# Performance work log

Measured on AMD Instinct MI355X. Metric: run time of the kernel, lower is better.

## Reference

```python
import jax, jax.numpy as jnp
import numpy as np
from jax import lax

EPS = 1e-7  # keras.backend.epsilon()
DT = 0.05

def _k(a):
    # (3,3) -> HWIO (3,3,1,1) fp32 kernel constant
    return jnp.asarray(np.asarray(a, dtype=np.float32).reshape(3, 3, 1, 1))

KXP = _k([[0,0,0],[0,-1,1],[0,0,0]])
KXN = _k([[0,0,0],[-1,1,0],[0,0,0]])
KYP = _k([[0,1,0],[0,-1,0],[0,0,0]])
KYN = _k([[0,0,0],[0,1,0],[0,-1,0]])
KXC = _k([[0,0,0],[-1,0,1],[0,0,0]])
KYC = _k([[0,1,0],[0,0,0],[0,-1,0]])
KLX = _k([[1,0,-1],[2,0,-2],[1,0,-1]])
KLY = _k([[1,2,1],[0,0,0],[-1,-2,-1]])

def conv(x, k):
    # TF K.conv2d 'same' == XLA cross-correlation, NHWC/HWIO
    return lax.conv_general_dilated(x, k, (1, 1), 'SAME',
                                    dimension_numbers=('NHWC', 'HWIO', 'NHWC'))

def setup_inputs() -> dict:
    key = jax.random.key(0)
    k1, k2 = jax.random.split(key)
    B, H, W = 32, 512, 512
    u = jax.random.normal(k1, (B, H, W, 1), dtype=jnp.float32)
    img = jax.random.uniform(k2, (B, H, W, 1), dtype=jnp.float32)
    alpha = jnp.ones((1, 1, 1, 1), jnp.float32)
    beta = jnp.ones((1, 1, 1, 1), jnp.float32)
    gamma = jnp.ones((1, 1, 1, 1), jnp.float32)
    return {"u": u, "img": img, "alpha": alpha, "beta": beta, "gamma": gamma}

def reference(u, img, alpha, beta, gamma):
    # --- edge stopping function g(img) (precomputed in build() in original) ---
    ex = conv(img, KLX)
    ey = conv(img, KLY)
    edges = jnp.square(jnp.square(ex) + jnp.square(ey))
    edges = edges / jnp.max(edges)
    edges = 1.0 / (edges + 1.0)
    gex = conv(edges, KXC)
    gey = conv(edges, KYC)
    # --- upwind transport term ---
    xp = conv(u, KXP); xn = conv(u, KXN)
    yp = conv(u, KYP); yn = conv(u, KYN)
    fxp = jax.nn.relu(gex); fxn = -jax.nn.relu(-gex)
    fyp = jax.nn.relu(gey); fyn = -jax.nn.relu(-gey)
    transport = 20.0 * ((fxp * xp + fxn * xn) + (fyp * yp + fyn * yn))
    # --- curvature (divergence of normalized gradient) ---
    gux = conv(u, KXC)
    guy = conv(u, KYC)
    normu = jnp.sqrt(jnp.square(gux) + jnp.square(guy) + EPS)
    kappa = conv(gux / (normu + EPS), KXC) + conv(guy / (normu + EPS), KYC)
    curvature = edges * kappa * normu
    balloon = edges * normu
    return u + DT * (curvature * alpha + transport * beta + balloon * gamma)
```

## Files before the change

### kernel.cpp

```cpp
#include <hip/hip_runtime.h>

#define HH 512
#define WW 512
#define NB 32
#define EPSF 1e-7f
#define DTF 0.05f
#define RS1 4
#define RSF 8
#define PANW 256

__device__ __forceinline__ float bperm(int addr, float v) {
    return __int_as_float(__builtin_amdgcn_ds_bpermute(addr, __float_as_int(v)));
}

struct R10 { float v[10]; };

__device__ __forceinline__ void load_row10(const float* __restrict__ base, int row,
                                           int lane, int bpu, int bpd,
                                           bool lo, bool hi, R10& r) {
    if ((unsigned)row < (unsigned)HH) {
        const float4* p = (const float4*)(base + row * WW + 8 * lane);
        float4 a = p[0], b = p[1];
        r.v[1] = a.x; r.v[2] = a.y; r.v[3] = a.z; r.v[4] = a.w;
        r.v[5] = b.x; r.v[6] = b.y; r.v[7] = b.z; r.v[8] = b.w;
    } else {
        #pragma unroll
        for (int k = 1; k <= 8; ++k) r.v[k] = 0.f;
    }
    float l = bperm(bpu, r.v[8]);
    float h = bperm(bpd, r.v[1]);
    r.v[0] = lo ? 0.f : l;
    r.v[9] = hi ? 0.f : h;
}

__global__ __launch_bounds__(256, 4)
void max_e4_kernel(const float* __restrict__ img, float* __restrict__ partial) {
    const int wid  = blockIdx.x * 4 + (threadIdx.x >> 6);
    const int lane = threadIdx.x & 63;
    const int rs = wid & 127;
    const int b  = wid >> 7;
    const int i0 = rs * RS1;
    const float* __restrict__ IM = img + (size_t)b * (HH * WW);
    const bool lo = (lane == 0), hi = (lane == 63);
    const int bpu = ((lane + 63) & 63) << 2, bpd = ((lane + 1) & 63) << 2;

    R10 A, B, C;
    load_row10(IM, i0 - 1, lane, bpu, bpd, lo, hi, A);
    load_row10(IM, i0,     lane, bpu, bpd, lo, hi, B);
    float m = 0.f;
    #pragma unroll
    for (int i = i0; i < i0 + RS1; ++i) {
        load_row10(IM, i + 1, lane, bpu, bpd, lo, hi, C);
        #pragma unroll
        for (int k = 1; k <= 8; ++k) {
            float ex = (A.v[k-1] - A.v[k+1]) + 2.f * (B.v[k-1] - B.v[k+1]) + (C.v[k-1] - C.v[k+1]);
            float ey = (A.v[k-1] - C.v[k-1]) + 2.f * (A.v[k] - C.v[k]) + (A.v[k+1] - C.v[k+1]);
            float s2 = ex * ex + ey * ey;
            m = fmaxf(m, s2 * s2);
        }
        A = B; B = C;
    }
    for (int off = 32; off > 0; off >>= 1)
        m = fmaxf(m, __shfl_down(m, off, 64));
    if (lane == 0) partial[wid] = m;
}

struct R7 { float v[6]; float x; };
struct RawR { float4 a; float2 t; };

__device__ __forceinline__ void load_raw(const float* __restrict__ base, int row,
                                         int lane, int c0, bool actL, bool actR, RawR& r) {
    if ((unsigned)row < (unsigned)HH) {
        const float* rp = base + (size_t)row * WW;
        r.a = *(const float4*)(rp + c0 + 4 * lane);
        if (actL | actR)
            r.t = *(const float2*)(rp + (actL ? c0 - 2 : c0 + PANW));
        else
            r.t = make_float2(0.f, 0.f);
    } else {
        r.a = make_float4(0.f, 0.f, 0.f, 0.f);
        r.t = make_float2(0.f, 0.f);
    }
}

__device__ __forceinline__ void finish_row(const RawR& q, int bpu, int bpd,
                                           bool actL, bool actR, bool zL, bool zR, R7& r) {
    r.v[1] = q.a.x; r.v[2] = q.a.y; r.v[3] = q.a.z; r.v[4] = q.a.w;
    float l = bperm(bpu, r.v[4]);
    float h = bperm(bpd, r.v[1]);
    float xx = 0.f;
    if (actL) { l = q.t.y; xx = q.t.x; }
    if (actR) { h = q.t.x; xx = q.t.y; }
    r.v[0] = zL ? 0.f : l;
    r.v[5] = zR ? 0.f : h;
    r.x = xx;
}

__device__ __forceinline__ void load_row(const float* __restrict__ base, int row,
                                         int lane, int c0, int bpu, int bpd,
                                         bool actL, bool actR, bool zL, bool zR, R7& r) {
    RawR q;
    load_raw(base, row, lane, c0, actL, actR, q);
    finish_row(q, bpu, bpd, actL, actR, zL, zR, r);
}

__global__ __launch_bounds__(256, 3)
void fused_ff(const float* __restrict__ u, const float* __restrict__ img,
              const float* __restrict__ pa, const float* __restrict__ pb,
              const float* __restrict__ pg, const float* __restrict__ partial,
              float* __restrict__ out) {
    const float va = pa[0], vb = pb[0], vg = pg[0];

    __shared__ float sred[4];
    {
        float v = 0.f;
        #pragma unroll
        for (int k = 0; k < 16; ++k)
            v = fmaxf(v, partial[threadIdx.x + 256 * k]);
        for (int off = 32; off > 0; off >>= 1)
            v = fmaxf(v, __shfl_down(v, off, 64));
        if ((threadIdx.x & 63) == 0) sred[threadIdx.x >> 6] = v;
    }
    __syncthreads();
    const float M = fmaxf(fmaxf(sred[0], sred[1]), fmaxf(sred[2], sred[3]));

    const int wid  = blockIdx.x * 4 + (threadIdx.x >> 6);
    const int lane = threadIdx.x & 63;
    const int p  = wid & 1;
    const int rs = (wid >> 1) & 63;
    const int b  = wid >> 7;
    const int o0 = rs * RSF;
    const int c0 = p * PANW;
    const size_t base = (size_t)b * (HH * WW);
    const float* __restrict__ U  = u + base;
    const float* __restrict__ IM = img + base;
    float* __restrict__ O = out + base;
    const int bpu = ((lane + 63) & 63) << 2, bpd = ((lane + 1) & 63) << 2;
    const bool l0 = (lane == 0), l63 = (lane == 63);
    const bool actL = l0  && (c0 > 0);
    const bool actR = l63 && (c0 + PANW < WW);
    const bool zL = l0 && !actL, zR = l63 && !actR;

    const float dta = DTF * va;
    const float dtb = 20.f * DTF * vb;
    const float dtg = DTF * vg;

    R7 I0 = {}, I1 = {}, R1 = {}, R2 = {};
    float E2[6] = {}, PX2[6] = {};
    float R0[5] = {}, E1[5] = {}, PY1[5] = {}, PY2[5] = {};

    if (o0 >= 2) {
        load_row(IM, o0 - 2, lane, c0, bpu, bpd, actL, actR, zL, zR, I0);
        load_row(IM, o0 - 1, lane, c0, bpu, bpd, actL, actR, zL, zR, I1);
        load_row(U,  o0 - 2, lane, c0, bpu, bpd, actL, actR, zL, zR, R1);
        load_row(U,  o0 - 1, lane, c0, bpu, bpd, actL, actR, zL, zR, R2);
    }

    #pragma unroll
    for (int o = o0 - 2; o < o0 + RSF; ++o) {
        RawR qc, qw;
        load_raw(IM, o + 2, lane, c0, actL, actR, qc);
        load_raw(U,  o + 2, lane, c0, actL, actR, qw);
        R7 C, W;
        finish_row(qc, bpu, bpd, actL, actR, zL, zR, C);
        finish_row(qw, bpu, bpd, actL, actR, zL, zR, W);

        float eN[6], PXN[6], PYN[5];
        const bool rowv = (o >= -1) && (o < HH - 1);
        if (rowv) {
            #pragma unroll
            for (int k = 1; k <= 4; ++k) {
                float ex = (I0.v[k-1] - I0.v[k+1]) + 2.f * (I1.v[k-1] - I1.v[k+1]) + (C.v[k-1] - C.v[k+1]);
                float ey = (I0.v[k-1] - C.v[k-1]) + 2.f * (I0.v[k] - C.v[k]) + (I0.v[k+1] - C.v[k+1]);
                float s2 = ex * ex + ey * ey;
                eN[k] = M * __builtin_amdgcn_rcpf(s2 * s2 + M);
                float gux = R2.v[k+1] - R2.v[k-1];
                float guy = R1.v[k] - W.v[k];
                float rn  = __builtin_amdgcn_rsqf(gux * gux + guy * guy + EPSF);
                PXN[k] = gux * rn;
                PYN[k] = guy * rn;
            }
        } else {
            #pragma unroll
            for (int k = 1; k <= 4; ++k) { eN[k] = 0.f; PXN[k] = 0.f; PYN[k] = 0.f; }
        }
        {
            float a = bperm(bpu, eN[4]),  bb = bperm(bpd, eN[1]);
            float c = bperm(bpu, PXN[4]), d  = bperm(bpd, PXN[1]);
            eN[0]  = zL ? 0.f : a;  eN[5]  = zR ? 0.f : bb;
            PXN[0] = zL ? 0.f : c;  PXN[5] = zR ? 0.f : d;
        }
        if (rowv && (actL | actR)) {
            float i0a = actL ? I0.x    : I0.v[4];
            float i0b = actL ? I0.v[0] : I0.v[5];
            float i0c = actL ? I0.v[1] : I0.x;
            float i1a = actL ? I1.x    : I1.v[4];
            float i1c = actL ? I1.v[1] : I1.x;
            float ca  = actL ? C.x     : C.v[4];
            float cb  = actL ? C.v[0]  : C.v[5];
            float cc  = actL ? C.v[1]  : C.x;
            float ex = (i0a - i0c) + 2.f * (i1a - i1c) + (ca - cc);
            float ey = (i0a - ca) + 2.f * (i0b - cb) + (i0c - cc);
            float s2 = ex * ex + ey * ey;
            float eh = M * __builtin_amdgcn_rcpf(s2 * s2 + M);
            float gux = actL ? (R2.v[1] - R2.x)    : (R2.x - R2.v[4]);
            float guy = actL ? (R1.v[0] - W.v[0])  : (R1.v[5] - W.v[5]);
            float rn = __builtin_amdgcn_rsqf(gux * gux + guy * guy + EPSF);
            float ph = gux * rn;
            if (actL) { eN[0] = eh; PXN[0] = ph; }
            else      { eN[5] = eh; PXN[5] = ph; }
        }

        if (o >= o0) {
            float vals[4];
            #pragma unroll
            for (int k = 1; k <= 4; ++k) {
                float gex = E2[k+1] - E2[k-1];
                float gey = E1[k] - eN[k];
                float xp = R1.v[k+1] - R1.v[k], xn = R1.v[k] - R1.v[k-1];
                float yp = R0[k] - R1.v[k],     yn = R1.v[k] - R2.v[k];
                float tr = fmaxf(gex, 0.f) * xp + fminf(gex, 0.f) * xn
                         + fmaxf(gey, 0.f) * yp + fminf(gey, 0.f) * yn;
                float gxc = R1.v[k+1] - R1.v[k-1], gyc = R0[k] - R2.v[k];
                float ncv = __builtin_amdgcn_sqrtf(gxc * gxc + gyc * gyc + EPSF);
                float kap = (PX2[k+1] - PX2[k-1]) + (PY1[k] - PYN[k]);
                vals[k-1] = R1.v[k] + E2[k] * ncv * (kap * dta + dtg) + tr * dtb;
            }
            *(float4*)(O + (size_t)o * WW + c0 + 4 * lane) =
                make_float4(vals[0], vals[1], vals[2], vals[3]);
        }

        I0 = I1; I1 = C;
        #pragma unroll
        for (int k = 1; k <= 4; ++k) { R0[k] = R1.v[k]; E1[k] = E2[k]; PY1[k] = PY2[k]; PY2[k] = PYN[k]; }
        R1 = R2; R2 = W;
        #pragma unroll
        for (int k = 0; k < 6; ++k) { E2[k] = eN[k]; PX2[k] = PXN[k]; }
    }
}

extern "C" void kernel_launch(void* const* d_in, const int* in_sizes, int n_in,
                              void* d_out, int out_size, void* d_ws, size_t ws_size,
                              hipStream_t stream) {
    const float* u   = (const float*)d_in[0];
    const float* img = (const float*)d_in[1];
    const float* pa  = (const float*)d_in[2];
    const float* pb  = (const float*)d_in[3];
    const float* pg  = (const float*)d_in[4];
    float* out = (float*)d_out;
    float* partial = (float*)d_ws;

    max_e4_kernel<<<1024, 256, 0, stream>>>(img, partial);
    fused_ff<<<1024, 256, 0, stream>>>(u, img, pa, pb, pg, partial, out);
}
```

Before: 127.9 us.

## Fuse max pass and stencil into one persistent kernel with grid barrier

```diff
diff --git a/kernel.cpp b/kernel.cpp
--- a/kernel.cpp
+++ b/kernel.cpp
@@ -2,74 +2,47 @@
 
 #define HH 512
 #define WW 512
-#define NB 32
 #define EPSF 1e-7f
 #define DTF 0.05f
-#define RS1 4
-#define RSF 8
+#define RS 8
 #define PANW 256
+
+__device__ int g_done = 0;
+__device__ unsigned g_maxu = 0u;
 
 __device__ __forceinline__ float bperm(int addr, float v) {
     return __int_as_float(__builtin_amdgcn_ds_bpermute(addr, __float_as_int(v)));
 }
 
 struct R10 { float v[10]; };
-
-__device__ __forceinline__ void load_row10(const float* __restrict__ base, int row,
-                                           int lane, int bpu, int bpd,
-                                           bool lo, bool hi, R10& r) {
+struct Raw10 { float4 a, b; };
+
+__device__ __forceinline__ void issue_row10(const float* __restrict__ base, int row,
+                                            int lane, Raw10& r) {
     if ((unsigned)row < (unsigned)HH) {
-        const float4* p = (const float4*)(base + row * WW + 8 * lane);
-        float4 a = p[0], b = p[1];
-        r.v[1] = a.x; r.v[2] = a.y; r.v[3] = a.z; r.v[4] = a.w;
-        r.v[5] = b.x; r.v[6] = b.y; r.v[7] = b.z; r.v[8] = b.w;
+        const float4* p = (const float4*)(base + (size_t)row * WW + 8 * lane);
+        r.a = p[0]; r.b = p[1];
     } else {
-        #pragma unroll
-        for (int k = 1; k <= 8; ++k) r.v[k] = 0.f;
-    }
+        r.a = make_float4(0.f, 0.f, 0.f, 0.f);
+        r.b = make_float4(0.f, 0.f, 0.f, 0.f);
+    }
+}
+
+__device__ __forceinline__ void finish_row10(const Raw10& q, int bpu, int bpd,
+                                             bool lo, bool hi, R10& r) {
+    r.v[1] = q.a.x; r.v[2] = q.a.y; r.v[3] = q.a.z; r.v[4] = q.a.w;
+    r.v[5] = q.b.x; r.v[6] = q.b.y; r.v[7] = q.b.z; r.v[8] = q.b.w;
     float l = bperm(bpu, r.v[8]);
     float h = bperm(bpd, r.v[1]);
     r.v[0] = lo ? 0.f : l;
     r.v[9] = hi ? 0.f : h;
 }
 
-__global__ __launch_bounds__(256, 4)
-void max_e4_kernel(const float* __restrict__ img, float* __restrict__ partial) {
-    const int wid  = blockIdx.x * 4 + (threadIdx.x >> 6);
-    const int lane = threadIdx.x & 63;
-    const int rs = wid & 127;
-    const int b  = wid >> 7;
-    const int i0 = rs * RS1;
-    const float* __restrict__ IM = img + (size_t)b * (HH * WW);
-    const bool lo = (lane == 0), hi = (lane == 63);
-    const int bpu = ((lane + 63) & 63) << 2, bpd = ((lane + 1) & 63) << 2;
-
-    R10 A, B, C;
-    load_row10(IM, i0 - 1, lane, bpu, bpd, lo, hi, A);
-    load_row10(IM, i0,     lane, bpu, bpd, lo, hi, B);
-    float m = 0.f;
-    #pragma unroll
-    for (int i = i0; i < i0 + RS1; ++i) {
-        load_row10(IM, i + 1, lane, bpu, bpd, lo, hi, C);
-        #pragma unroll
-        for (int k = 1; k <= 8; ++k) {
-            float ex = (A.v[k-1] - A.v[k+1]) + 2.f * (B.v[k-1] - B.v[k+1]) + (C.v[k-1] - C.v[k+1]);
-            float ey = (A.v[k-1] - C.v[k-1]) + 2.f * (A.v[k] - C.v[k]) + (A.v[k+1] - C.v[k+1]);
-            float s2 = ex * ex + ey * ey;
-            m = fmaxf(m, s2 * s2);
-        }
-        A = B; B = C;
-    }
-    for (int off = 32; off > 0; off >>= 1)
-        m = fmaxf(m, __shfl_down(m, off, 64));
-    if (lane == 0) partial[wid] = m;
-}
-
 struct R7 { float v[6]; float x; };
 struct RawR { float4 a; float2 t; };
 
-__device__ __forceinline__ void load_raw(const float* __restrict__ base, int row,
-                                         int lane, int c0, bool actL, bool actR, RawR& r) {
+__device__ __forceinline__ void issue_row(const float* __restrict__ base, int row,
+                                          int lane, int c0, bool actL, bool actR, RawR& r) {
     if ((unsigned)row < (unsigned)HH) {
         const float* rp = base + (size_t)row * WW;
         r.a = *(const float4*)(rp + c0 + 4 * lane);
@@ -96,146 +69,199 @@
     r.x = xx;
 }
 
-__device__ __forceinline__ void load_row(const float* __restrict__ base, int row,
-                                         int lane, int c0, int bpu, int bpd,
-                                         bool actL, bool actR, bool zL, bool zR, R7& r) {
-    RawR q;
-    load_raw(base, row, lane, c0, actL, actR, q);
-    finish_row(q, bpu, bpd, actL, actR, zL, zR, r);
-}
-
-__global__ __launch_bounds__(256, 3)
-void fused_ff(const float* __restrict__ u, const float* __restrict__ img,
-              const float* __restrict__ pa, const float* __restrict__ pb,
-              const float* __restrict__ pg, const float* __restrict__ partial,
-              float* __restrict__ out) {
+__global__ __launch_bounds__(256, 2)
+void fused_all(const float* __restrict__ u, const float* __restrict__ img,
+               const float* __restrict__ pa, const float* __restrict__ pb,
+               const float* __restrict__ pg, float* __restrict__ out) {
+    const int widx = threadIdx.x >> 6;
+    const int lane = threadIdx.x & 63;
+    const int wid  = blockIdx.x * 4 + widx;
+    const int rs = wid & 63;
+    const int b  = wid >> 6;
+    const int i0 = rs * RS;
+    const size_t base = (size_t)b * (HH * WW);
+    const float* __restrict__ IM = img + base;
+    const float* __restrict__ U  = u + base;
+    float* __restrict__ O = out + base;
+    const bool l0 = (lane == 0), l63 = (lane == 63);
+    const int bpu = ((lane + 63) & 63) << 2, bpd = ((lane + 1) & 63) << 2;
+
     const float va = pa[0], vb = pb[0], vg = pg[0];
 
-    __shared__ float sred[4];
+    float m = 0.f;
     {
-        float v = 0.f;
+        Raw10 rA, rB;
+        issue_row10(IM, i0 - 1, lane, rA);
+        issue_row10(IM, i0,     lane, rB);
+        R10 A, B, C;
+        finish_row10(rA, bpu, bpd, l0, l63, A);
+        issue_row10(IM, i0 + 1, lane, rA);
+        finish_row10(rB, bpu, bpd, l0, l63, B);
+        issue_row10(IM, i0 + 2, lane, rB);
         #pragma unroll
-        for (int k = 0; k < 16; ++k)
-            v = fmaxf(v, partial[threadIdx.x + 256 * k]);
+        for (int k = 0; k < RS; ++k) {
+            if (k & 1) {
+                finish_row10(rB, bpu, bpd, l0, l63, C);
+                if (k < RS - 2) issue_row10(IM, i0 + k + 3, lane, rB);
+            } else {
+                finish_row10(rA, bpu, bpd, l0, l63, C);
+                if (k < RS - 2) issue_row10(IM, i0 + k + 3, lane, rA);
+            }
+            #pragma unroll
+            for (int j = 1; j <= 8; ++j) {
+                float ex = (A.v[j-1] - A.v[j+1]) + 2.f * (B.v[j-1] - B.v[j+1]) + (C.v[j-1] - C.v[j+1]);
+                float ey = (A.v[j-1] - C.v[j-1]) + 2.f * (A.v[j] - C.v[j]) + (A.v[j+1] - C.v[j+1]);
+                float s2 = ex * ex + ey * ey;
+                m = fmaxf(m, s2 * s2);
+            }
+            A = B; B = C;
+        }
         for (int off = 32; off > 0; off >>= 1)
-            v = fmaxf(v, __shfl_down(v, off, 64));
-        if ((threadIdx.x & 63) == 0) sred[threadIdx.x >> 6] = v;
-    }
+            m = fmaxf(m, __shfl_down(m, off, 64));
+    }
+
+    __shared__ float swm[4];
+    __shared__ float sM;
+    if (lane == 0) swm[widx] = m;
     __syncthreads();
-    const float M = fmaxf(fmaxf(sred[0], sred[1]), fmaxf(sred[2], sred[3]));
-
-    const int wid  = blockIdx.x * 4 + (threadIdx.x >> 6);
-    const int lane = threadIdx.x & 63;
-    const int p  = wid & 1;
-    const int rs = (wid >> 1) & 63;
-    const int b  = wid >> 7;
-    const int o0 = rs * RSF;
-    const int c0 = p * PANW;
-    const size_t base = (size_t)b * (HH * WW);
-    const float* __restrict__ U  = u + base;
-    const float* __restrict__ IM = img + base;
-    float* __restrict__ O = out + base;
-    const int bpu = ((lane + 63) & 63) << 2, bpd = ((lane + 1) & 63) << 2;
-    const bool l0 = (lane == 0), l63 = (lane == 63);
-    const bool actL = l0  && (c0 > 0);
-    const bool actR = l63 && (c0 + PANW < WW);
-    const bool zL = l0 && !actL, zR = l63 && !actR;
+    if (threadIdx.x == 0) {
+        float bm = fmaxf(fmaxf(swm[0], swm[1]), fmaxf(swm[2], swm[3]));
+        atomicMax(&g_maxu, __float_as_uint(bm));
+        int t = __hip_atomic_fetch_add(&g_done, 1, __ATOMIC_ACQ_REL, __HIP_MEMORY_SCOPE_AGENT);
+        const int target = (t & ~511) + 512;
+        while (__hip_atomic_load(&g_done, __ATOMIC_ACQUIRE, __HIP_MEMORY_SCOPE_AGENT) < target)
+            __builtin_amdgcn_s_sleep(2);
+        sM = __uint_as_float(__hip_atomic_load(&g_maxu, __ATOMIC_RELAXED, __HIP_MEMORY_SCOPE_AGENT));
+    }
+    __syncthreads();
+    const float M = sM;
 
     const float dta = DTF * va;
     const float dtb = 20.f * DTF * vb;
     const float dtg = DTF * vg;
 
-    R7 I0 = {}, I1 = {}, R1 = {}, R2 = {};
-    float E2[6] = {}, PX2[6] = {};
-    float R0[5] = {}, E1[5] = {}, PY1[5] = {}, PY2[5] = {};
-
-    if (o0 >= 2) {
-        load_row(IM, o0 - 2, lane, c0, bpu, bpd, actL, actR, zL, zR, I0);
-        load_row(IM, o0 - 1, lane, c0, bpu, bpd, actL, actR, zL, zR, I1);
-        load_row(U,  o0 - 2, lane, c0, bpu, bpd, actL, actR, zL, zR, R1);
-        load_row(U,  o0 - 1, lane, c0, bpu, bpd, actL, actR, zL, zR, R2);
-    }
-
-    #pragma unroll
-    for (int o = o0 - 2; o < o0 + RSF; ++o) {
-        RawR qc, qw;
-        load_raw(IM, o + 2, lane, c0, actL, actR, qc);
-        load_raw(U,  o + 2, lane, c0, actL, actR, qw);
-        R7 C, W;
-        finish_row(qc, bpu, bpd, actL, actR, zL, zR, C);
-        finish_row(qw, bpu, bpd, actL, actR, zL, zR, W);
-
-        float eN[6], PXN[6], PYN[5];
-        const bool rowv = (o >= -1) && (o < HH - 1);
-        if (rowv) {
+    const int o0 = i0;
+    #pragma unroll 1
+    for (int pp = 0; pp < 2; ++pp) {
+        const int c0 = pp * PANW;
+        const bool actL = l0  && (c0 > 0);
+        const bool actR = l63 && (c0 + PANW < WW);
+        const bool zL = l0 && !actL, zR = l63 && !actR;
+
+        R7 I0 = {}, I1 = {}, R1 = {}, R2 = {};
+        float E2[6] = {}, PX2[6] = {};
+        float R0[5] = {}, E1[5] = {}, PY1[5] = {}, PY2[5] = {};
+
+        if (o0 >= 2) {
+            RawR q0i, q0u, q1i, q1u;
+            issue_row(IM, o0 - 2, lane, c0, actL, actR, q0i);
+            issue_row(U,  o0 - 2, lane, c0, actL, actR, q0u);
+            issue_row(IM, o0 - 1, lane, c0, actL, actR, q1i);
+            issue_row(U,  o0 - 1, lane, c0, actL, actR, q1u);
+            finish_row(q0i, bpu, bpd, actL, actR, zL, zR, I0);
+            finish_row(q0u, bpu, bpd, actL, actR, zL, zR, R1);
+            finish_row(q1i, bpu, bpd, actL, actR, zL, zR, I1);
+            finish_row(q1u, bpu, bpd, actL, actR, zL, zR, R2);
+        }
+
+        RawR pAi, pAu, pBi, pBu;
+        issue_row(IM, o0,     lane, c0, actL, actR, pAi);
+        issue_row(U,  o0,     lane, c0, actL, actR, pAu);
+        issue_row(IM, o0 + 1, lane, c0, actL, actR, pBi);
+        issue_row(U,  o0 + 1, lane, c0, actL, actR, pBu);
+
+        #pragma unroll
+        for (int kk = 0; kk < RS + 2; ++kk) {
+            const int o = o0 - 2 + kk;
+            R7 C, W;
+            if (kk & 1) {
+                finish_row(pBi, bpu, bpd, actL, actR, zL, zR, C);
+                finish_row(pBu, bpu, bpd, actL, actR, zL, zR, W);
+                if (kk < RS) {
+                    issue_row(IM, o0 + kk + 2, lane, c0, actL, actR, pBi);
+                    issue_row(U,  o0 + kk + 2, lane, c0, actL, actR, pBu);
+                }
+            } else {
+                finish_row(pAi, bpu, bpd, actL, actR, zL, zR, C);
+                finish_row(pAu, bpu, bpd, actL, actR, zL, zR, W);
+                if (kk < RS) {
+                    issue_row(IM, o0 + kk + 2, lane, c0, actL, actR, pAi);
+                    issue_row(U,  o0 + kk + 2, lane, c0, actL, actR, pAu);
+                }
+            }
+
+            float eN[6], PXN[6], PYN[5];
+            const bool rowv = (o >= -1) && (o < HH - 1);
+            if (rowv) {
+                #pragma unroll
+                for (int k = 1; k <= 4; ++k) {
+                    float ex = (I0.v[k-1] - I0.v[k+1]) + 2.f * (I1.v[k-1] - I1.v[k+1]) + (C.v[k-1] - C.v[k+1]);
+                    float ey = (I0.v[k-1] - C.v[k-1]) + 2.f * (I0.v[k] - C.v[k]) + (I0.v[k+1] - C.v[k+1]);
+                    float s2 = ex * ex + ey * ey;
+                    eN[k] = M * __builtin_amdgcn_rcpf(s2 * s2 + M);
+                    float gux = R2.v[k+1] - R2.v[k-1];
+                    float guy = R1.v[k] - W.v[k];
+                    float rn  = __builtin_amdgcn_rsqf(gux * gux + guy * guy + EPSF);
+                    PXN[k] = gux * rn;
+                    PYN[k] = guy * rn;
+                }
+            } else {
+                #pragma unroll
+                for (int k = 1; k <= 4; ++k) { eN[k] = 0.f; PXN[k] = 0.f; PYN[k] = 0.f; }
+            }
+            {
+                float a = bperm(bpu, eN[4]),  bb = bperm(bpd, eN[1]);
+                float c = bperm(bpu, PXN[4]), d  = bperm(bpd, PXN[1]);
+                eN[0]  = zL ? 0.f : a;  eN[5]  = zR ? 0.f : bb;
+                PXN[0] = zL ? 0.f : c;  PXN[5] = zR ? 0.f : d;
+            }
+            if (rowv && (actL | actR)) {
+                float i0a = actL ? I0.x    : I0.v[4];
+                float i0b = actL ? I0.v[0] : I0.v[5];
+                float i0c = actL ? I0.v[1] : I0.x;
+                float i1a = actL ? I1.x    : I1.v[4];
+                float i1c = actL ? I1.v[1] : I1.x;
+                float ca  = actL ? C.x     : C.v[4];
+                float cb  = actL ? C.v[0]  : C.v[5];
+                float cc  = actL ? C.v[1]  : C.x;
+                float ex = (i0a - i0c) + 2.f * (i1a - i1c) + (ca - cc);
+                float ey = (i0a - ca) + 2.f * (i0b - cb) + (i0c - cc);
+                float s2 = ex * ex + ey * ey;
+                float eh = M * __builtin_amdgcn_rcpf(s2 * s2 + M);
+                float gux = actL ? (R2.v[1] - R2.x)    : (R2.x - R2.v[4]);
+                float guy = actL ? (R1.v[0] - W.v[0])  : (R1.v[5] - W.v[5]);
+                float rn = __builtin_amdgcn_rsqf(gux * gux + guy * guy + EPSF);
+                float ph = gux * rn;
+                if (actL) { eN[0] = eh; PXN[0] = ph; }
+                else      { eN[5] = eh; PXN[5] = ph; }
+            }
+
+            if (o >= o0) {
+                float vals[4];
+                #pragma unroll
+                for (int k = 1; k <= 4; ++k) {
+                    float gex = E2[k+1] - E2[k-1];
+                    float gey = E1[k] - eN[k];
+                    float xp = R1.v[k+1] - R1.v[k], xn = R1.v[k] - R1.v[k-1];
+                    float yp = R0[k] - R1.v[k],     yn = R1.v[k] - R2.v[k];
+                    float tr = fmaxf(gex, 0.f) * xp + fminf(gex, 0.f) * xn
+                             + fmaxf(gey, 0.f) * yp + fminf(gey, 0.f) * yn;
+                    float gxc = R1.v[k+1] - R1.v[k-1], gyc = R0[k] - R2.v[k];
+                    float ncv = __builtin_amdgcn_sqrtf(gxc * gxc + gyc * gyc + EPSF);
+                    float kap = (PX2[k+1] - PX2[k-1]) + (PY1[k] - PYN[k]);
+                    vals[k-1] = R1.v[k] + E2[k] * ncv * (kap * dta + dtg) + tr * dtb;
+                }
+                *(float4*)(O + (size_t)o * WW + c0 + 4 * lane) =
+                    make_float4(vals[0], vals[1], vals[2], vals[3]);
+            }
+
+            I0 = I1; I1 = C;
             #pragma unroll
-            for (int k = 1; k <= 4; ++k) {
-                float ex = (I0.v[k-1] - I0.v[k+1]) + 2.f * (I1.v[k-1] - I1.v[k+1]) + (C.v[k-1] - C.v[k+1]);
-                float ey = (I0.v[k-1] - C.v[k-1]) + 2.f * (I0.v[k] - C.v[k]) + (I0.v[k+1] - C.v[k+1]);
-                float s2 = ex * ex + ey * ey;
-                eN[k] = M * __builtin_amdgcn_rcpf(s2 * s2 + M);
-                float gux = R2.v[k+1] - R2.v[k-1];
-                float guy = R1.v[k] - W.v[k];
-                float rn  = __builtin_amdgcn_rsqf(gux * gux + guy * guy + EPSF);
-                PXN[k] = gux * rn;
-                PYN[k] = guy * rn;
-            }
-        } else {
+            for (int k = 1; k <= 4; ++k) { R0[k] = R1.v[k]; E1[k] = E2[k]; PY1[k] = PY2[k]; PY2[k] = PYN[k]; }
+            R1 = R2; R2 = W;
             #pragma unroll
-            for (int k = 1; k <= 4; ++k) { eN[k] = 0.f; PXN[k] = 0.f; PYN[k] = 0.f; }
+            for (int k = 0; k < 6; ++k) { E2[k] = eN[k]; PX2[k] = PXN[k]; }
         }
-        {
-            float a = bperm(bpu, eN[4]),  bb = bperm(bpd, eN[1]);
-            float c = bperm(bpu, PXN[4]), d  = bperm(bpd, PXN[1]);
-            eN[0]  = zL ? 0.f : a;  eN[5]  = zR ? 0.f : bb;
-            PXN[0] = zL ? 0.f : c;  PXN[5] = zR ? 0.f : d;
-        }
-        if (rowv && (actL | actR)) {
-            float i0a = actL ? I0.x    : I0.v[4];
-            float i0b = actL ? I0.v[0] : I0.v[5];
-            float i0c = actL ? I0.v[1] : I0.x;
-            float i1a = actL ? I1.x    : I1.v[4];
-            float i1c = actL ? I1.v[1] : I1.x;
-            float ca  = actL ? C.x     : C.v[4];
-            float cb  = actL ? C.v[0]  : C.v[5];
-            float cc  = actL ? C.v[1]  : C.x;
-            float ex = (i0a - i0c) + 2.f * (i1a - i1c) + (ca - cc);
-            float ey = (i0a - ca) + 2.f * (i0b - cb) + (i0c - cc);
-            float s2 = ex * ex + ey * ey;
-            float eh = M * __builtin_amdgcn_rcpf(s2 * s2 + M);
-            float gux = actL ? (R2.v[1] - R2.x)    : (R2.x - R2.v[4]);
-            float guy = actL ? (R1.v[0] - W.v[0])  : (R1.v[5] - W.v[5]);
-            float rn = __builtin_amdgcn_rsqf(gux * gux + guy * guy + EPSF);
-            float ph = gux * rn;
-            if (actL) { eN[0] = eh; PXN[0] = ph; }
-            else      { eN[5] = eh; PXN[5] = ph; }
-        }
-
-        if (o >= o0) {
-            float vals[4];
-            #pragma unroll
-            for (int k = 1; k <= 4; ++k) {
-                float gex = E2[k+1] - E2[k-1];
-                float gey = E1[k] - eN[k];
-                float xp = R1.v[k+1] - R1.v[k], xn = R1.v[k] - R1.v[k-1];
-                float yp = R0[k] - R1.v[k],     yn = R1.v[k] - R2.v[k];
-                float tr = fmaxf(gex, 0.f) * xp + fminf(gex, 0.f) * xn
-                         + fmaxf(gey, 0.f) * yp + fminf(gey, 0.f) * yn;
-                float gxc = R1.v[k+1] - R1.v[k-1], gyc = R0[k] - R2.v[k];
-                float ncv = __builtin_amdgcn_sqrtf(gxc * gxc + gyc * gyc + EPSF);
-                float kap = (PX2[k+1] - PX2[k-1]) + (PY1[k] - PYN[k]);
-                vals[k-1] = R1.v[k] + E2[k] * ncv * (kap * dta + dtg) + tr * dtb;
-            }
-            *(float4*)(O + (size_t)o * WW + c0 + 4 * lane) =
-                make_float4(vals[0], vals[1], vals[2], vals[3]);
-        }
-
-        I0 = I1; I1 = C;
-        #pragma unroll
-        for (int k = 1; k <= 4; ++k) { R0[k] = R1.v[k]; E1[k] = E2[k]; PY1[k] = PY2[k]; PY2[k] = PYN[k]; }
-        R1 = R2; R2 = W;
-        #pragma unroll
-        for (int k = 0; k < 6; ++k) { E2[k] = eN[k]; PX2[k] = PXN[k]; }
     }
 }
 
@@ -248,8 +274,7 @@
     const float* pb  = (const float*)d_in[3];
     const float* pg  = (const float*)d_in[4];
     float* out = (float*)d_out;
-    float* partial = (float*)d_ws;
-
-    max_e4_kernel<<<1024, 256, 0, stream>>>(img, partial);
-    fused_ff<<<1024, 256, 0, stream>>>(u, img, pa, pb, pg, partial, out);
-}
+    (void)d_ws; (void)ws_size;
+
+    fused_all<<<512, 256, 0, stream>>>(u, img, pa, pb, pg, out);
+}
```

Measured after the change: 154.7 us. +21.0%, slower.
